# Optimization experiments

Hardware: AMD Instinct MI355X
Metric: run time of the kernel (lower is better)

Reference implementation:

```python
import jax, jax.numpy as jnp
import numpy as np

N_NODES = 100000

def gcn_conv(x, edge_index, W, b):
    # GCNConv with normalize=True and self-loops:
    # out = D^{-1/2} (A + I) D^{-1/2} (x W) + b
    h = x @ W                                   # [N, out]
    src, dst = edge_index[0], edge_index[1]
    deg = jax.ops.segment_sum(jnp.ones(src.shape[0], h.dtype), dst,
                              num_segments=N_NODES) + 1.0  # +1 for self loop
    dinv = jax.lax.rsqrt(deg)
    norm = dinv[src] * dinv[dst]                # [E]
    agg = jax.ops.segment_sum(h[src] * norm[:, None], dst,
                              num_segments=N_NODES)        # [N, out]
    agg = agg + h * (1.0 / deg)[:, None]        # self-loop term: norm_ii = 1/deg_i
    return agg + b


def setup_inputs() -> dict:
    key = jax.random.key(0)
    k0, k1, k2, k3 = jax.random.split(key, 4)
    N, E, F_IN, H, C = N_NODES, 1600000, 256, 128, 40
    x = jax.random.normal(k0, (N, F_IN), dtype=jnp.float32)
    edge_index = jax.random.randint(k1, (2, E), 0, N, dtype=jnp.int64)
    W1 = jax.random.normal(k2, (F_IN, H), dtype=jnp.float32) * (1.0 / np.sqrt(F_IN))
    b1 = jnp.zeros((H,), jnp.float32)
    W2 = jax.random.normal(k3, (H, C), dtype=jnp.float32) * (1.0 / np.sqrt(H))
    b2 = jnp.zeros((C,), jnp.float32)
    return {"x": x, "edge_index": edge_index, "W1": W1, "b1": b1, "W2": W2, "b2": b2}


def reference(x, edge_index, W1, b1, W2, b2):
    # layer 1 + ReLU (dropout = identity in eval mode)
    h = jax.nn.relu(gcn_conv(x, edge_index, W1, b1))
    # final layer (no activation)
    return gcn_conv(h, edge_index, W2, b2)
```

## Files before the change

### kernel.cpp

```cpp
#include <hip/hip_runtime.h>
#include <hip/hip_bf16.h>


#define FIN 256
#define HDIM 128
#define CDIM 40
#define CAP 8192
#define EC 8192

typedef __attribute__((ext_vector_type(8))) short bf16x8;
typedef __attribute__((ext_vector_type(4))) float f32x4;
typedef __attribute__((ext_vector_type(2))) float f32x2;

__device__ inline short f2bf(float f) {
    unsigned u = __float_as_uint(f);
    unsigned r = (u + 0x7FFFu + ((u >> 16) & 1u)) >> 16;
    return (short)r;
}
__device__ inline float bflo(unsigned u) { return __uint_as_float(u << 16); }
__device__ inline float bfhi(unsigned u) { return __uint_as_float(u & 0xFFFF0000u); }
__device__ inline f32x2 unpk(unsigned u) { return (f32x2){bflo(u), bfhi(u)}; }

__global__ __launch_bounds__(1024) void scatter_k(const int* __restrict__ ei, int* __restrict__ gcnt,
                                                  int* __restrict__ bmem, int E, int NBUCK) {
    __shared__ int hist[512];
    __shared__ int base[512];
    const int tid = threadIdx.x;
    for (int t = tid; t < NBUCK; t += 1024) hist[t] = 0;
    __syncthreads();
    const int e0 = blockIdx.x * EC;
    const int e1 = min(E, e0 + EC);
    for (int e = e0 + tid; e < e1; e += 1024) atomicAdd(&hist[ei[E + e] >> 8], 1);
    __syncthreads();
    for (int t = tid; t < NBUCK; t += 1024) base[t] = atomicAdd(&gcnt[t], hist[t]);
    __syncthreads();
    for (int e = e0 + tid; e < e1; e += 1024) {
        int s = ei[e];
        int d = ei[E + e];
        int b = d >> 8;
        int pos = atomicAdd(&base[b], 1);
        bmem[b * CAP + pos] = s | ((d & 255) << 20);
    }
}

__global__ __launch_bounds__(256) void p2_build_k(const int* __restrict__ bmem, const int* __restrict__ bcnt,
                                                  int* __restrict__ csr, int2* __restrict__ nseg,
                                                  float* __restrict__ dinv, float* __restrict__ invd,
                                                  const float* __restrict__ W1, const float* __restrict__ W2,
                                                  short* __restrict__ W1T, short* __restrict__ W2T, int N) {
    __shared__ int hist[256], cur[256], sc[256];
    __shared__ int stage[CAP];
    const int b = blockIdx.x;
    const int tid = threadIdx.x;

    for (int idx = b * 256 + tid; idx < FIN * HDIM + 48 * HDIM; idx += gridDim.x * 256) {
        if (idx < FIN * HDIM) {
            int k = idx >> 7, n = idx & 127;
            W1T[n * FIN + k] = f2bf(W1[idx]);
        } else {
            int j = idx - FIN * HDIM;
            int c = j >> 7, k = j & 127;
            W2T[j] = (c < CDIM) ? f2bf(W2[k * CDIM + c]) : (short)0;
        }
    }

    int cnt = bcnt[b];
    if (cnt > CAP) cnt = CAP;
    const int* src = bmem + b * CAP;
    hist[tid] = 0;
    __syncthreads();
    for (int j = tid; j < cnt; j += 256) atomicAdd(&hist[src[j] >> 20], 1);
    __syncthreads();
    int v = hist[tid];
    sc[tid] = v;
    __syncthreads();
    for (int off = 1; off < 256; off <<= 1) {
        int t = (tid >= off) ? sc[tid - off] : 0;
        __syncthreads();
        sc[tid] += t;
        __syncthreads();
    }
    int excl = sc[tid] - v;
    cur[tid] = excl;
    int i = b * 256 + tid;
    if (i < N) {
        nseg[i] = make_int2(b * CAP + excl, v);
        float dg = (float)(v + 1);
        dinv[i] = rsqrtf(dg);
        invd[i] = 1.0f / dg;
    }
    __syncthreads();
    for (int j = tid; j < cnt; j += 256) {
        int rec = src[j];
        int pos = atomicAdd(&cur[rec >> 20], 1);
        stage[pos] = rec & 0xFFFFF;
    }
    __syncthreads();
    int* dst = csr + b * CAP;
    for (int j = tid; j < cnt; j += 256) dst[j] = stage[j];
}

#define LDSTRIDE 40
__global__ __launch_bounds__(256) void gemm1_mfma_k(const float* __restrict__ X,
                                                    const short* __restrict__ W1T,
                                                    short* __restrict__ T1b, int N) {
    __shared__ short As[128 * LDSTRIDE];
    __shared__ short Bs[128 * LDSTRIDE];
    const int tid = threadIdx.x;
    const int lane = tid & 63;
    const int wid = tid >> 6;
    const int w0 = wid & 1, w1 = wid >> 1;
    const int quad = lane >> 4;
    const int l16 = lane & 15;
    const int rowbase = blockIdx.x * 128;
    const int sr = tid >> 1;
    const int sh = tid & 1;

    f32x4 acc[4][4];
#pragma unroll
    for (int a = 0; a < 4; a++)
#pragma unroll
        for (int b = 0; b < 4; b++) acc[a][b] = (f32x4){0.f, 0.f, 0.f, 0.f};

    const int arow = min(rowbase + sr, N - 1);
    const float* xsrc = X + (size_t)arow * FIN + sh * 16;
    const int4* bsrc = (const int4*)(W1T + (size_t)sr * FIN + sh * 16);

    for (int k0 = 0; k0 < FIN; k0 += 32) {
        float vals[16];
        *(float4*)&vals[0]  = *(const float4*)(xsrc + k0);
        *(float4*)&vals[4]  = *(const float4*)(xsrc + k0 + 4);
        *(float4*)&vals[8]  = *(const float4*)(xsrc + k0 + 8);
        *(float4*)&vals[12] = *(const float4*)(xsrc + k0 + 12);
        short tmp[16];
#pragma unroll
        for (int c = 0; c < 16; c++) tmp[c] = f2bf(vals[c]);
        ((int4*)&As[sr * LDSTRIDE + sh * 16])[0] = ((int4*)tmp)[0];
        ((int4*)&As[sr * LDSTRIDE + sh * 16])[1] = ((int4*)tmp)[1];
        int4 b0 = bsrc[k0 >> 3];
        int4 b1 = bsrc[(k0 >> 3) + 1];
        ((int4*)&Bs[sr * LDSTRIDE + sh * 16])[0] = b0;
        ((int4*)&Bs[sr * LDSTRIDE + sh * 16])[1] = b1;
        __syncthreads();

        bf16x8 afr[4], bfr[4];
#pragma unroll
        for (int mt = 0; mt < 4; mt++)
            afr[mt] = *(const bf16x8*)&As[(w1 * 64 + mt * 16 + l16) * LDSTRIDE + quad * 8];
#pragma unroll
        for (int nt = 0; nt < 4; nt++)
            bfr[nt] = *(const bf16x8*)&Bs[(w0 * 64 + nt * 16 + l16) * LDSTRIDE + quad * 8];
#pragma unroll
        for (int mt = 0; mt < 4; mt++)
#pragma unroll
            for (int nt = 0; nt < 4; nt++)
                acc[mt][nt] = __builtin_amdgcn_mfma_f32_16x16x32_bf16(afr[mt], bfr[nt], acc[mt][nt], 0, 0, 0);
        __syncthreads();
    }
#pragma unroll
    for (int mt = 0; mt < 4; mt++) {
#pragma unroll
        for (int r = 0; r < 4; r++) {
            int row = rowbase + w1 * 64 + mt * 16 + quad * 4 + r;
            if (row < N) {
#pragma unroll
                for (int nt = 0; nt < 4; nt++) {
                    int col = w0 * 64 + nt * 16 + l16;
                    T1b[(size_t)row * HDIM + col] = f2bf(acc[mt][nt][r]);
                }
            }
        }
    }
}

__global__ __launch_bounds__(256) void agg1_k(const short* __restrict__ T1b, const int2* __restrict__ nseg,
                                              const int* __restrict__ csr, const float* __restrict__ dinv,
                                              const float* __restrict__ invd, const float* __restrict__ b1,
                                              unsigned* __restrict__ Hb, int N) {
    const int lane = threadIdx.x & 63;
    const int quad = lane >> 4;
    const int ql = lane & 15;
    const int i = blockIdx.x * 4 + (threadIdx.x >> 6);
    if (i >= N) return;
    const int2 sg = nseg[i];
    const int e0 = sg.x, deg = sg.y;
    int sv = 0; float wv = 0.f;
    if (lane < deg) { sv = csr[e0 + lane]; wv = dinv[sv]; }

    const uint4* rowp = (const uint4*)T1b;
    f32x2 acc[4];
#pragma unroll
    for (int t = 0; t < 4; t++) acc[t] = (f32x2){0.f, 0.f};

    const int dmain = deg < 64 ? deg : 64;
    for (int j = 0; j < dmain; j += 16) {
        const int i0 = j + quad, i1 = j + 4 + quad, i2 = j + 8 + quad, i3 = j + 12 + quad;
        int s0 = __shfl(sv, i0); int s1 = __shfl(sv, i1);
        int s2 = __shfl(sv, i2); int s3 = __shfl(sv, i3);
        float w0 = __shfl(wv, i0); float w1 = __shfl(wv, i1);
        float w2 = __shfl(wv, i2); float w3 = __shfl(wv, i3);
        w0 = (i0 < dmain) ? w0 : 0.f;
        w1 = (i1 < dmain) ? w1 : 0.f;
        w2 = (i2 < dmain) ? w2 : 0.f;
        w3 = (i3 < dmain) ? w3 : 0.f;
        uint4 u0 = rowp[s0 * 16 + ql];
        uint4 u1 = rowp[s1 * 16 + ql];
        uint4 u2 = rowp[s2 * 16 + ql];
        uint4 u3 = rowp[s3 * 16 + ql];
        f32x2 W0 = (f32x2){w0, w0}, W1v = (f32x2){w1, w1}, W2v = (f32x2){w2, w2}, W3v = (f32x2){w3, w3};
        acc[0] += W0 * unpk(u0.x) + W1v * unpk(u1.x) + W2v * unpk(u2.x) + W3v * unpk(u3.x);
        acc[1] += W0 * unpk(u0.y) + W1v * unpk(u1.y) + W2v * unpk(u2.y) + W3v * unpk(u3.y);
        acc[2] += W0 * unpk(u0.z) + W1v * unpk(u1.z) + W2v * unpk(u2.z) + W3v * unpk(u3.z);
        acc[3] += W0 * unpk(u0.w) + W1v * unpk(u1.w) + W2v * unpk(u2.w) + W3v * unpk(u3.w);
    }
    const int eEnd = e0 + deg;
    for (int e = e0 + 64; e < eEnd; e += 4) {
        int idx = e + quad;
        int cl = idx < eEnd ? idx : eEnd - 1;
        int sj = csr[cl];
        float wj = (idx < eEnd) ? dinv[sj] : 0.f;
        uint4 u = rowp[sj * 16 + ql];
        f32x2 Wj = (f32x2){wj, wj};
        acc[0] += Wj * unpk(u.x);
        acc[1] += Wj * unpk(u.y);
        acc[2] += Wj * unpk(u.z);
        acc[3] += Wj * unpk(u.w);
    }
#pragma unroll
    for (int t = 0; t < 4; t++) {
        acc[t].x += __shfl_xor(acc[t].x, 16); acc[t].y += __shfl_xor(acc[t].y, 16);
        acc[t].x += __shfl_xor(acc[t].x, 32); acc[t].y += __shfl_xor(acc[t].y, 32);
    }
    const float di = dinv[i], sf = invd[i];
    uint4 us = rowp[i * 16 + ql];
    float4 bA = *(const float4*)(b1 + ql * 8);
    float4 bB = *(const float4*)(b1 + ql * 8 + 4);
    float o0 = fmaxf(bA.x + sf * bflo(us.x) + di * acc[0].x, 0.f);
    float o1 = fmaxf(bA.y + sf * bfhi(us.x) + di * acc[0].y, 0.f);
    float o2 = fmaxf(bA.z + sf * bflo(us.y) + di * acc[1].x, 0.f);
    float o3 = fmaxf(bA.w + sf * bfhi(us.y) + di * acc[1].y, 0.f);
    float o4 = fmaxf(bB.x + sf * bflo(us.z) + di * acc[2].x, 0.f);
    float o5 = fmaxf(bB.y + sf * bfhi(us.z) + di * acc[2].y, 0.f);
    float o6 = fmaxf(bB.z + sf * bflo(us.w) + di * acc[3].x, 0.f);
    float o7 = fmaxf(bB.w + sf * bfhi(us.w) + di * acc[3].y, 0.f);
    uint4 pk;
    pk.x = ((unsigned)(unsigned short)f2bf(o0)) | (((unsigned)(unsigned short)f2bf(o1)) << 16);
    pk.y = ((unsigned)(unsigned short)f2bf(o2)) | (((unsigned)(unsigned short)f2bf(o3)) << 16);
    pk.z = ((unsigned)(unsigned short)f2bf(o4)) | (((unsigned)(unsigned short)f2bf(o5)) << 16);
    pk.w = ((unsigned)(unsigned short)f2bf(o6)) | (((unsigned)(unsigned short)f2bf(o7)) << 16);
    if (quad == 0) ((uint4*)(Hb + (size_t)i * 64))[ql] = pk;
}

__global__ __launch_bounds__(256) void gemm2_mfma_k(const short* __restrict__ Hb,
                                                    const short* __restrict__ W2T,
                                                    short* __restrict__ T2b, int N) {
    __shared__ short As[128 * LDSTRIDE];
    __shared__ short Bs[48 * LDSTRIDE];
    const int tid = threadIdx.x;
    const int lane = tid & 63;
    const int wid = tid >> 6;
    const int quad = lane >> 4;
    const int l16 = lane & 15;
    const int rowbase = blockIdx.x * 128;
    const int sr = tid >> 1;
    const int sh = tid & 1;

    f32x4 acc[2][3];
#pragma unroll
    for (int a = 0; a < 2; a++)
#pragma unroll
        for (int b = 0; b < 3; b++) acc[a][b] = (f32x4){0.f, 0.f, 0.f, 0.f};

    const int arow = min(rowbase + sr, N - 1);
    const int4* asrc = (const int4*)(Hb + (size_t)arow * HDIM + sh * 16);
    const int br = tid >> 1, bh = tid & 1;
    const int4* bsrc = (const int4*)(W2T + br * HDIM + bh * 16);

    for (int k0 = 0; k0 < HDIM; k0 += 32) {
        int4 a0 = asrc[k0 >> 3];
        int4 a1 = asrc[(k0 >> 3) + 1];
        ((int4*)&As[sr * LDSTRIDE + sh * 16])[0] = a0;
        ((int4*)&As[sr * LDSTRIDE + sh * 16])[1] = a1;
        if (tid < 96) {
            int4 b0 = bsrc[k0 >> 3];
            int4 b1 = bsrc[(k0 >> 3) + 1];
            ((int4*)&Bs[br * LDSTRIDE + bh * 16])[0] = b0;
            ((int4*)&Bs[br * LDSTRIDE + bh * 16])[1] = b1;
        }
        __syncthreads();
        bf16x8 afr[2], bfr[3];
#pragma unroll
        for (int mt = 0; mt < 2; mt++)
            afr[mt] = *(const bf16x8*)&As[(wid * 32 + mt * 16 + l16) * LDSTRIDE + quad * 8];
#pragma unroll
        for (int nt = 0; nt < 3; nt++)
            bfr[nt] = *(const bf16x8*)&Bs[(nt * 16 + l16) * LDSTRIDE + quad * 8];
#pragma unroll
        for (int mt = 0; mt < 2; mt++)
#pragma unroll
            for (int nt = 0; nt < 3; nt++)
                acc[mt][nt] = __builtin_amdgcn_mfma_f32_16x16x32_bf16(afr[mt], bfr[nt], acc[mt][nt], 0, 0, 0);
        __syncthreads();
    }
#pragma unroll
    for (int mt = 0; mt < 2; mt++) {
#pragma unroll
        for (int r = 0; r < 4; r++) {
            int row = rowbase + wid * 32 + mt * 16 + quad * 4 + r;
            if (row < N) {
#pragma unroll
                for (int nt = 0; nt < 3; nt++) {
                    int col = nt * 16 + l16;
                    T2b[(size_t)row * 48 + col] = f2bf(acc[mt][nt][r]);
                }
            }
        }
    }
}

__global__ __launch_bounds__(256) void agg2_k(const short* __restrict__ T2b, const int2* __restrict__ nseg,
                                              const int* __restrict__ csr, const float* __restrict__ dinv,
                                              const float* __restrict__ invd, const float* __restrict__ b2,
                                              float* __restrict__ OUT, int N) {
    const int lane = threadIdx.x & 63;
    const int oct = lane >> 3;
    const int olr = lane & 7;
    const int ol = olr < 6 ? olr : 5;
    const bool act = olr < 6;
    const int i = blockIdx.x * 4 + (threadIdx.x >> 6);
    if (i >= N) return;
    const int2 sg = nseg[i];
    const int e0 = sg.x, deg = sg.y;
    int sv = 0; float wv = 0.f;
    if (lane < deg) { sv = csr[e0 + lane]; wv = dinv[sv]; }

    const uint4* rowp = (const uint4*)T2b;
    f32x2 acc[4];
#pragma unroll
    for (int t = 0; t < 4; t++) acc[t] = (f32x2){0.f, 0.f};

    const int dmain = deg < 64 ? deg : 64;
    for (int j = 0; j < dmain; j += 16) {
        const int i0 = j + oct, i1 = j + 8 + oct;
        int s0 = __shfl(sv, i0); int s1 = __shfl(sv, i1);
        float w0 = __shfl(wv, i0); float w1 = __shfl(wv, i1);
        w0 = (i0 < dmain && act) ? w0 : 0.f;
        w1 = (i1 < dmain && act) ? w1 : 0.f;
        uint4 u0 = rowp[s0 * 6 + ol];
        uint4 u1 = rowp[s1 * 6 + ol];
        f32x2 W0 = (f32x2){w0, w0}, W1v = (f32x2){w1, w1};
        acc[0] += W0 * unpk(u0.x) + W1v * unpk(u1.x);
        acc[1] += W0 * unpk(u0.y) + W1v * unpk(u1.y);
        acc[2] += W0 * unpk(u0.z) + W1v * unpk(u1.z);
        acc[3] += W0 * unpk(u0.w) + W1v * unpk(u1.w);
    }
    const int eEnd = e0 + deg;
    for (int e = e0 + 64; e < eEnd; e += 8) {
        int idx = e + oct;
        int cl = idx < eEnd ? idx : eEnd - 1;
        int sj = csr[cl];
        float wj = (idx < eEnd && act) ? dinv[sj] : 0.f;
        uint4 u = rowp[sj * 6 + ol];
        f32x2 Wj = (f32x2){wj, wj};
        acc[0] += Wj * unpk(u.x);
        acc[1] += Wj * unpk(u.y);
        acc[2] += Wj * unpk(u.z);
        acc[3] += Wj * unpk(u.w);
    }
#pragma unroll
    for (int t = 0; t < 4; t++) {
        acc[t].x += __shfl_xor(acc[t].x, 8);  acc[t].y += __shfl_xor(acc[t].y, 8);
        acc[t].x += __shfl_xor(acc[t].x, 16); acc[t].y += __shfl_xor(acc[t].y, 16);
        acc[t].x += __shfl_xor(acc[t].x, 32); acc[t].y += __shfl_xor(acc[t].y, 32);
    }
    if (oct == 0 && olr < 5) {
        const float di = dinv[i], sf = invd[i];
        uint4 us = rowp[i * 6 + olr];
        float4 bA = *(const float4*)(b2 + olr * 8);
        float4 bB = *(const float4*)(b2 + olr * 8 + 4);
        float4 oA, oB;
        oA.x = bA.x + sf * bflo(us.x) + di * acc[0].x;
        oA.y = bA.y + sf * bfhi(us.x) + di * acc[0].y;
        oA.z = bA.z + sf * bflo(us.y) + di * acc[1].x;
        oA.w = bA.w + sf * bfhi(us.y) + di * acc[1].y;
        oB.x = bB.x + sf * bflo(us.z) + di * acc[2].x;
        oB.y = bB.y + sf * bfhi(us.z) + di * acc[2].y;
        oB.z = bB.z + sf * bflo(us.w) + di * acc[3].x;
        oB.w = bB.w + sf * bfhi(us.w) + di * acc[3].y;
        *(float4*)(OUT + (size_t)i * CDIM + olr * 8) = oA;
        *(float4*)(OUT + (size_t)i * CDIM + olr * 8 + 4) = oB;
    }
}

extern "C" void kernel_launch(void* const* d_in, const int* in_sizes, int n_in,
                              void* d_out, int out_size, void* d_ws, size_t ws_size,
                              hipStream_t stream) {
    const float* x   = (const float*)d_in[0];
    const int*   ei  = (const int*)d_in[1];
    const float* W1  = (const float*)d_in[2];
    const float* b1  = (const float*)d_in[3];
    const float* W2  = (const float*)d_in[4];
    const float* b2  = (const float*)d_in[5];
    float*       out = (float*)d_out;

    const int Hd  = in_sizes[3];
    const int Fin = in_sizes[2] / Hd;
    const int N   = in_sizes[0] / Fin;
    const int E   = in_sizes[1] / 2;

    const int NBUCK = (N + 255) / 256;
    const int NB1   = (E + EC - 1) / EC;

    char* base = (char*)d_ws;
    size_t off = 0;
    auto alloc = [&](size_t bytes) -> void* {
        void* p = base + off;
        off += (bytes + 255) & ~(size_t)255;
        return p;
    };
    size_t bmemB = (size_t)NBUCK * CAP * 4;
    size_t t1bB  = (size_t)N * HDIM * 2;
    size_t regA  = bmemB > t1bB ? bmemB : t1bB;
    char* pA = (char*)alloc(regA);
    int*   bmem = (int*)pA;
    short* t1b  = (short*)pA;

    int*      gcnt = (int*)alloc((size_t)NBUCK * 4);
    int*      csr  = (int*)alloc((size_t)NBUCK * CAP * 4);
    int2*     nseg = (int2*)alloc((size_t)N * 8);
    float*    dinv = (float*)alloc((size_t)N * 4);
    float*    invd = (float*)alloc((size_t)N * 4);
    short*    W1T  = (short*)alloc((size_t)HDIM * FIN * 2);
    short*    W2T  = (short*)alloc((size_t)48 * HDIM * 2);
    unsigned* hb   = (unsigned*)alloc((size_t)N * HDIM * 2);
    short*    t2b  = (short*)alloc((size_t)N * 48 * 2);

    hipMemsetAsync(gcnt, 0, (size_t)NBUCK * 4, stream);
    scatter_k<<<NB1, 1024, 0, stream>>>(ei, gcnt, bmem, E, NBUCK);
    p2_build_k<<<NBUCK, 256, 0, stream>>>(bmem, gcnt, csr, nseg, dinv, invd, W1, W2, W1T, W2T, N);

    gemm1_mfma_k<<<(N + 127) / 128, 256, 0, stream>>>(x, W1T, t1b, N);
    agg1_k<<<(N + 3) / 4, 256, 0, stream>>>(t1b, nseg, csr, dinv, invd, b1, hb, N);
    gemm2_mfma_k<<<(N + 127) / 128, 256, 0, stream>>>((const short*)hb, W2T, t2b, N);
    agg2_k<<<(N + 3) / 4, 256, 0, stream>>>(t2b, nseg, csr, dinv, invd, b2, out, N);
}
```

Before: 334.1 us.

## Quantize layer-1 hidden features to per-row int8 for aggregation gather

New measurement: 321.7 us. -3.7%, faster.

```diff
diff --git a/kernel.cpp b/kernel.cpp
--- a/kernel.cpp
+++ b/kernel.cpp
@@ -20,6 +20,10 @@
 __device__ inline float bflo(unsigned u) { return __uint_as_float(u << 16); }
 __device__ inline float bfhi(unsigned u) { return __uint_as_float(u & 0xFFFF0000u); }
 __device__ inline f32x2 unpk(unsigned u) { return (f32x2){bflo(u), bfhi(u)}; }
+__device__ inline float ub0(unsigned u) { return (float)(u & 255u); }
+__device__ inline float ub1(unsigned u) { return (float)((u >> 8) & 255u); }
+__device__ inline float ub2(unsigned u) { return (float)((u >> 16) & 255u); }
+__device__ inline float ub3(unsigned u) { return (float)(u >> 24); }
 
 __global__ __launch_bounds__(1024) void scatter_k(const int* __restrict__ ei, int* __restrict__ gcnt,
                                                   int* __restrict__ bmem, int E, int NBUCK) {
@@ -103,9 +107,13 @@
 #define LDSTRIDE 40
 __global__ __launch_bounds__(256) void gemm1_mfma_k(const float* __restrict__ X,
                                                     const short* __restrict__ W1T,
-                                                    short* __restrict__ T1b, int N) {
-    __shared__ short As[128 * LDSTRIDE];
-    __shared__ short Bs[128 * LDSTRIDE];
+                                                    const float* __restrict__ dinv,
+                                                    unsigned char* __restrict__ T1q,
+                                                    float* __restrict__ scl,
+                                                    float* __restrict__ wsc, int N) {
+    __shared__ short SH[128 * LDSTRIDE * 2];
+    short* As = SH;
+    short* Bs = SH + 128 * LDSTRIDE;
     const int tid = threadIdx.x;
     const int lane = tid & 63;
     const int wid = tid >> 6;
@@ -157,24 +165,60 @@
                 acc[mt][nt] = __builtin_amdgcn_mfma_f32_16x16x32_bf16(afr[mt], bfr[nt], acc[mt][nt], 0, 0, 0);
         __syncthreads();
     }
+
+    unsigned char* qbuf = (unsigned char*)SH;
+    float* rmaxb = (float*)((char*)SH + 16384);
 #pragma unroll
     for (int mt = 0; mt < 4; mt++) {
 #pragma unroll
         for (int r = 0; r < 4; r++) {
-            int row = rowbase + w1 * 64 + mt * 16 + quad * 4 + r;
-            if (row < N) {
-#pragma unroll
-                for (int nt = 0; nt < 4; nt++) {
-                    int col = w0 * 64 + nt * 16 + l16;
-                    T1b[(size_t)row * HDIM + col] = f2bf(acc[mt][nt][r]);
-                }
+            float m = fabsf(acc[mt][0][r]);
+            m = fmaxf(m, fabsf(acc[mt][1][r]));
+            m = fmaxf(m, fabsf(acc[mt][2][r]));
+            m = fmaxf(m, fabsf(acc[mt][3][r]));
+#pragma unroll
+            for (int off = 1; off < 16; off <<= 1) m = fmaxf(m, __shfl_xor(m, off));
+            rmaxb[w0 * 128 + w1 * 64 + mt * 16 + quad * 4 + r] = m;
+        }
+    }
+    __syncthreads();
+    if (tid < 128) {
+        int grow = rowbase + tid;
+        if (grow < N) {
+            float rv = fmaxf(rmaxb[tid], rmaxb[128 + tid]);
+            float s = rv * (1.f / 127.f);
+            scl[grow] = s;
+            wsc[grow] = s * dinv[grow];
+        }
+    }
+#pragma unroll
+    for (int mt = 0; mt < 4; mt++) {
+#pragma unroll
+        for (int r = 0; r < 4; r++) {
+            const int row = w1 * 64 + mt * 16 + quad * 4 + r;
+            float rv = fmaxf(rmaxb[row], rmaxb[128 + row]);
+            float qinv = rv > 0.f ? 127.f / rv : 0.f;
+#pragma unroll
+            for (int nt = 0; nt < 4; nt++) {
+                int qi = (int)rintf(acc[mt][nt][r] * qinv) + 128;
+                qi = qi < 0 ? 0 : (qi > 255 ? 255 : qi);
+                qbuf[row * 128 + w0 * 64 + nt * 16 + l16] = (unsigned char)qi;
             }
         }
     }
-}
-
-__global__ __launch_bounds__(256) void agg1_k(const short* __restrict__ T1b, const int2* __restrict__ nseg,
-                                              const int* __restrict__ csr, const float* __restrict__ dinv,
+    __syncthreads();
+#pragma unroll
+    for (int it = 0; it < 4; it++) {
+        int idx = tid + it * 256;
+        int row = idx >> 3;
+        if (rowbase + row < N)
+            ((uint4*)(T1q + (size_t)(rowbase + row) * 128))[idx & 7] = ((const uint4*)qbuf)[idx];
+    }
+}
+
+__global__ __launch_bounds__(256) void agg1_k(const unsigned char* __restrict__ T1q, const int2* __restrict__ nseg,
+                                              const int* __restrict__ csr, const float* __restrict__ wsc,
+                                              const float* __restrict__ scl, const float* __restrict__ dinv,
                                               const float* __restrict__ invd, const float* __restrict__ b1,
                                               unsigned* __restrict__ Hb, int N) {
     const int lane = threadIdx.x & 63;
@@ -185,10 +229,13 @@
     const int2 sg = nseg[i];
     const int e0 = sg.x, deg = sg.y;
     int sv = 0; float wv = 0.f;
-    if (lane < deg) { sv = csr[e0 + lane]; wv = dinv[sv]; }
-
-    const uint4* rowp = (const uint4*)T1b;
-    f32x2 acc[4];
+    if (lane < deg) { sv = csr[e0 + lane]; wv = wsc[sv]; }
+
+    const uint2* rowp = (const uint2*)T1q;
+    uint2 us = rowp[i * 16 + ql];
+    const float sscale = scl[i];
+
+    f32x2 acc[4]; float asum = 0.f;
 #pragma unroll
     for (int t = 0; t < 4; t++) acc[t] = (f32x2){0.f, 0.f};
 
@@ -203,46 +250,56 @@
         w1 = (i1 < dmain) ? w1 : 0.f;
         w2 = (i2 < dmain) ? w2 : 0.f;
         w3 = (i3 < dmain) ? w3 : 0.f;
-        uint4 u0 = rowp[s0 * 16 + ql];
-        uint4 u1 = rowp[s1 * 16 + ql];
-        uint4 u2 = rowp[s2 * 16 + ql];
-        uint4 u3 = rowp[s3 * 16 + ql];
+        uint2 u0 = rowp[s0 * 16 + ql];
+        uint2 u1 = rowp[s1 * 16 + ql];
+        uint2 u2 = rowp[s2 * 16 + ql];
+        uint2 u3 = rowp[s3 * 16 + ql];
+        asum += w0 + w1 + w2 + w3;
         f32x2 W0 = (f32x2){w0, w0}, W1v = (f32x2){w1, w1}, W2v = (f32x2){w2, w2}, W3v = (f32x2){w3, w3};
-        acc[0] += W0 * unpk(u0.x) + W1v * unpk(u1.x) + W2v * unpk(u2.x) + W3v * unpk(u3.x);
-        acc[1] += W0 * unpk(u0.y) + W1v * unpk(u1.y) + W2v * unpk(u2.y) + W3v * unpk(u3.y);
-        acc[2] += W0 * unpk(u0.z) + W1v * unpk(u1.z) + W2v * unpk(u2.z) + W3v * unpk(u3.z);
-        acc[3] += W0 * unpk(u0.w) + W1v * unpk(u1.w) + W2v * unpk(u2.w) + W3v * unpk(u3.w);
+        acc[0] += W0 * (f32x2){ub0(u0.x), ub1(u0.x)} + W1v * (f32x2){ub0(u1.x), ub1(u1.x)}
+                + W2v * (f32x2){ub0(u2.x), ub1(u2.x)} + W3v * (f32x2){ub0(u3.x), ub1(u3.x)};
+        acc[1] += W0 * (f32x2){ub2(u0.x), ub3(u0.x)} + W1v * (f32x2){ub2(u1.x), ub3(u1.x)}
+                + W2v * (f32x2){ub2(u2.x), ub3(u2.x)} + W3v * (f32x2){ub2(u3.x), ub3(u3.x)};
+        acc[2] += W0 * (f32x2){ub0(u0.y), ub1(u0.y)} + W1v * (f32x2){ub0(u1.y), ub1(u1.y)}
+                + W2v * (f32x2){ub0(u2.y), ub1(u2.y)} + W3v * (f32x2){ub0(u3.y), ub1(u3.y)};
+        acc[3] += W0 * (f32x2){ub2(u0.y), ub3(u0.y)} + W1v * (f32x2){ub2(u1.y), ub3(u1.y)}
+                + W2v * (f32x2){ub2(u2.y), ub3(u2.y)} + W3v * (f32x2){ub2(u3.y), ub3(u3.y)};
     }
     const int eEnd = e0 + deg;
     for (int e = e0 + 64; e < eEnd; e += 4) {
         int idx = e + quad;
         int cl = idx < eEnd ? idx : eEnd - 1;
         int sj = csr[cl];
-        float wj = (idx < eEnd) ? dinv[sj] : 0.f;
-        uint4 u = rowp[sj * 16 + ql];
+        float wj = (idx < eEnd) ? wsc[sj] : 0.f;
+        uint2 u = rowp[sj * 16 + ql];
+        asum += wj;
         f32x2 Wj = (f32x2){wj, wj};
-        acc[0] += Wj * unpk(u.x);
-        acc[1] += Wj * unpk(u.y);
-        acc[2] += Wj * unpk(u.z);
-        acc[3] += Wj * unpk(u.w);
+        acc[0] += Wj * (f32x2){ub0(u.x), ub1(u.x)};
+        acc[1] += Wj * (f32x2){ub2(u.x), ub3(u.x)};
+        acc[2] += Wj * (f32x2){ub0(u.y), ub1(u.y)};
+        acc[3] += Wj * (f32x2){ub2(u.y), ub3(u.y)};
     }
 #pragma unroll
     for (int t = 0; t < 4; t++) {
         acc[t].x += __shfl_xor(acc[t].x, 16); acc[t].y += __shfl_xor(acc[t].y, 16);
         acc[t].x += __shfl_xor(acc[t].x, 32); acc[t].y += __shfl_xor(acc[t].y, 32);
     }
-    const float di = dinv[i], sf = invd[i];
-    uint4 us = rowp[i * 16 + ql];
+    asum += __shfl_xor(asum, 16);
+    asum += __shfl_xor(asum, 32);
+
+    const float di = dinv[i];
+    const float sf2 = invd[i] * sscale;
+    const float K = -128.f * (sf2 + di * asum);
     float4 bA = *(const float4*)(b1 + ql * 8);
     float4 bB = *(const float4*)(b1 + ql * 8 + 4);
-    float o0 = fmaxf(bA.x + sf * bflo(us.x) + di * acc[0].x, 0.f);
-    float o1 = fmaxf(bA.y + sf * bfhi(us.x) + di * acc[0].y, 0.f);
-    float o2 = fmaxf(bA.z + sf * bflo(us.y) + di * acc[1].x, 0.f);
-    float o3 = fmaxf(bA.w + sf * bfhi(us.y) + di * acc[1].y, 0.f);
-    float o4 = fmaxf(bB.x + sf * bflo(us.z) + di * acc[2].x, 0.f);
-    float o5 = fmaxf(bB.y + sf * bfhi(us.z) + di * acc[2].y, 0.f);
-    float o6 = fmaxf(bB.z + sf * bflo(us.w) + di * acc[3].x, 0.f);
-    float o7 = fmaxf(bB.w + sf * bfhi(us.w) + di * acc[3].y, 0.f);
+    float o0 = fmaxf(bA.x + sf2 * ub0(us.x) + di * acc[0].x + K, 0.f);
+    float o1 = fmaxf(bA.y + sf2 * ub1(us.x) + di * acc[0].y + K, 0.f);
+    float o2 = fmaxf(bA.z + sf2 * ub2(us.x) + di * acc[1].x + K, 0.f);
+    float o3 = fmaxf(bA.w + sf2 * ub3(us.x) + di * acc[1].y + K, 0.f);
+    float o4 = fmaxf(bB.x + sf2 * ub0(us.y) + di * acc[2].x + K, 0.f);
+    float o5 = fmaxf(bB.y + sf2 * ub1(us.y) + di * acc[2].y + K, 0.f);
+    float o6 = fmaxf(bB.z + sf2 * ub2(us.y) + di * acc[3].x + K, 0.f);
+    float o7 = fmaxf(bB.w + sf2 * ub3(us.y) + di * acc[3].y + K, 0.f);
     uint4 pk;
     pk.x = ((unsigned)(unsigned short)f2bf(o0)) | (((unsigned)(unsigned short)f2bf(o1)) << 16);
     pk.y = ((unsigned)(unsigned short)f2bf(o2)) | (((unsigned)(unsigned short)f2bf(o3)) << 16);
@@ -419,17 +476,19 @@
         return p;
     };
     size_t bmemB = (size_t)NBUCK * CAP * 4;
-    size_t t1bB  = (size_t)N * HDIM * 2;
-    size_t regA  = bmemB > t1bB ? bmemB : t1bB;
+    size_t t1qB  = (size_t)N * 128;
+    size_t regA  = bmemB > t1qB ? bmemB : t1qB;
     char* pA = (char*)alloc(regA);
-    int*   bmem = (int*)pA;
-    short* t1b  = (short*)pA;
+    int*           bmem = (int*)pA;
+    unsigned char* t1q  = (unsigned char*)pA;
 
     int*      gcnt = (int*)alloc((size_t)NBUCK * 4);
     int*      csr  = (int*)alloc((size_t)NBUCK * CAP * 4);
     int2*     nseg = (int2*)alloc((size_t)N * 8);
     float*    dinv = (float*)alloc((size_t)N * 4);
     float*    invd = (float*)alloc((size_t)N * 4);
+    float*    scl  = (float*)alloc((size_t)N * 4);
+    float*    wsc  = (float*)alloc((size_t)N * 4);
     short*    W1T  = (short*)alloc((size_t)HDIM * FIN * 2);
     short*    W2T  = (short*)alloc((size_t)48 * HDIM * 2);
     unsigned* hb   = (unsigned*)alloc((size_t)N * HDIM * 2);
@@ -439,8 +498,8 @@
     scatter_k<<<NB1, 1024, 0, stream>>>(ei, gcnt, bmem, E, NBUCK);
     p2_build_k<<<NBUCK, 256, 0, stream>>>(bmem, gcnt, csr, nseg, dinv, invd, W1, W2, W1T, W2T, N);
 
-    gemm1_mfma_k<<<(N + 127) / 128, 256, 0, stream>>>(x, W1T, t1b, N);
-    agg1_k<<<(N + 3) / 4, 256, 0, stream>>>(t1b, nseg, csr, dinv, invd, b1, hb, N);
+    gemm1_mfma_k<<<(N + 127) / 128, 256, 0, stream>>>(x, W1T, dinv, t1q, scl, wsc, N);
+    agg1_k<<<(N + 3) / 4, 256, 0, stream>>>(t1q, nseg, csr, wsc, scl, dinv, invd, b1, hb, N);
     gemm2_mfma_k<<<(N + 127) / 128, 256, 0, stream>>>((const short*)hb, W2T, t2b, N);
     agg2_k<<<(N + 3) / 4, 256, 0, stream>>>(t2b, nseg, csr, dinv, invd, b2, out, N);
 }
```
